# Performance work log

Measured on AMD Instinct MI355X. Metric: run time of the kernel, lower is better.

The kernel has to match this reference:

```python
import jax, jax.numpy as jnp
import numpy as np

N_NODES = 50000
N_EDGES = 800000
D_IN = 128
D_HID = 128
D_OUT = 128


def _sage_conv(x, row, col, Wl, Wr, b):
    # PyG SAGEConv (mean aggregation, root weight, bias):
    # out = mean_{j in N(i)} x_j @ Wl^T + x_i @ Wr^T + b
    n = x.shape[0]
    msg = x[col]                                            # [E, D] gather from source nodes
    agg = jax.ops.segment_sum(msg, row, num_segments=n)     # [N, D]
    deg = jax.ops.segment_sum(jnp.ones((row.shape[0],), x.dtype), row, num_segments=n)
    agg = agg / jnp.maximum(deg, 1.0)[:, None]
    return agg @ Wl.T + x @ Wr.T + b


def setup_inputs() -> dict:
    key = jax.random.key(0)
    ks = jax.random.split(key, 12)
    x = jax.random.normal(ks[0], (N_NODES, D_IN), dtype=jnp.float32)
    edge_row = jax.random.randint(ks[1], (N_EDGES,), 0, N_NODES)
    edge_col = jax.random.randint(ks[2], (N_EDGES,), 0, N_NODES)
    dims = [(D_HID, D_IN), (D_HID, D_HID), (D_OUT, D_HID)]
    inp = {"x": x, "edge_row": edge_row, "edge_col": edge_col}
    for i, (do, di) in enumerate(dims):
        s = 1.0 / np.sqrt(di)
        inp[f"Wl{i}"] = jax.random.uniform(ks[3 + 3 * i], (do, di), jnp.float32, -s, s)
        inp[f"Wr{i}"] = jax.random.uniform(ks[4 + 3 * i], (do, di), jnp.float32, -s, s)
        inp[f"b{i}"] = jax.random.uniform(ks[5 + 3 * i], (do,), jnp.float32, -s, s)
    return inp


def reference(x, edge_row, edge_col, Wl0, Wr0, b0, Wl1, Wr1, b1, Wl2, Wr2, b2):
    # Single branch (num_layers=[3]), use_res=True, dropout=0 (eval mode).
    params = [(Wl0, Wr0, b0), (Wl1, Wr1, b1), (Wl2, Wr2, b2)]
    x1 = _sage_conv(x, edge_row, edge_col, *params[0])
    for Wl, Wr, b in params[1:]:
        x2 = x1
        x1 = jax.nn.relu(x1)
        x1 = _sage_conv(x1, edge_row, edge_col, Wl, Wr, b) + x2
    # x_final = sum(branches) / number; one branch -> divide by 1
    return x1 / 1.0
```

## Files before the change

### kernel.cpp

```cpp
#include <hip/hip_runtime.h>

#define NN 50000
#define NE 800000
#define D  128

typedef _Float16 f16;
typedef _Float16 f16x4 __attribute__((ext_vector_type(4)));
typedef _Float16 f16x8 __attribute__((ext_vector_type(8)));
typedef float f32x4 __attribute__((ext_vector_type(4)));
typedef float f32x2 __attribute__((ext_vector_type(2)));
typedef unsigned short u16;
typedef unsigned int u32;
typedef unsigned char u8;

__global__ __launch_bounds__(256) void prep(
    const float* __restrict__ x, f16* __restrict__ xf, u8* __restrict__ xf8,
    const float* w0, const float* w1, const float* w2,
    const float* w3, const float* w4, const float* w5,
    f16* d0, f16* d1, f16* d2, f16* d3, f16* d4, f16* d5,
    int* __restrict__ deg) {
    int b = blockIdx.x;
    if (b < 6250) {
        int i = b * 256 + threadIdx.x;
        float4 v = ((const float4*)x)[i];
        f16x4 o = {(f16)v.x, (f16)v.y, (f16)v.z, (f16)v.w};
        ((f16x4*)xf)[i] = o;
        u32 lo = __builtin_amdgcn_cvt_pk_fp8_f32(v.x, v.y, 0, false);
        u32 pk = __builtin_amdgcn_cvt_pk_fp8_f32(v.z, v.w, lo, true);
        ((u32*)xf8)[i] = pk;
    } else if (b < 6346) {
        int wb = b - 6250;
        int mat = wb >> 4;
        const float* s; f16* d;
        switch (mat) {
            case 0: s = w0; d = d0; break; case 1: s = w1; d = d1; break;
            case 2: s = w2; d = d2; break; case 3: s = w3; d = d3; break;
            case 4: s = w4; d = d4; break; default: s = w5; d = d5; break;
        }
        int i = (wb & 15) * 256 + threadIdx.x;
        float4 v = ((const float4*)s)[i];
        f16x4 o = {(f16)v.x, (f16)v.y, (f16)v.z, (f16)v.w};
        ((f16x4*)d)[i] = o;
    } else {
        int i = (b - 6346) * 256 + threadIdx.x;
        if (i < NN) deg[i] = 0;
    }
}


__global__ __launch_bounds__(256) void count_deg_rank(
    const int* __restrict__ row, int* __restrict__ deg, u16* __restrict__ rank, int e) {
    int i = blockIdx.x * blockDim.x + threadIdx.x;
    if (i < e) rank[i] = (u16)atomicAdd(&deg[row[i]], 1);
}

__global__ void scan_partial(const int* __restrict__ deg, int* __restrict__ bsum, int n) {
    __shared__ int s[1024];
    int i = blockIdx.x * 1024 + threadIdx.x;
    s[threadIdx.x] = (i < n) ? deg[i] : 0;
    __syncthreads();
    for (int off = 512; off > 0; off >>= 1) {
        if (threadIdx.x < off) s[threadIdx.x] += s[threadIdx.x + off];
        __syncthreads();
    }
    if (threadIdx.x == 0) bsum[blockIdx.x] = s[0];
}

__global__ void scan_final(const int* __restrict__ deg, const int* __restrict__ bsum,
                           int* __restrict__ offsets, int n, int nb) {
    __shared__ int s[1024];
    __shared__ int base;
    if (threadIdx.x < 64) {
        int t = threadIdx.x;
        int v = (t < nb && t < (int)blockIdx.x) ? bsum[t] : 0;
#pragma unroll
        for (int m = 1; m < 64; m <<= 1) v += __shfl_xor(v, m, 64);
        if (t == 0) base = v;
    }
    int i = blockIdx.x * 1024 + threadIdx.x;
    int dv = (i < n) ? deg[i] : 0;
    s[threadIdx.x] = dv;
    __syncthreads();
    for (int off = 1; off < 1024; off <<= 1) {
        int t = (threadIdx.x >= (unsigned)off) ? s[threadIdx.x - off] : 0;
        __syncthreads();
        s[threadIdx.x] += t;
        __syncthreads();
    }
    if (i < n) {
        offsets[i + 1] = s[threadIdx.x] + base;
        if (i == 0) offsets[0] = 0;
    }
}

__global__ __launch_bounds__(256) void fill_csr(
    const int* __restrict__ row, const int* __restrict__ col,
    const u16* __restrict__ rank, const int* __restrict__ offsets,
    u16* __restrict__ csr_col, int e) {
    int i = blockIdx.x * blockDim.x + threadIdx.x;
    if (i < e) {
        int p = offsets[row[i]] + (int)rank[i];
        csr_col[p] = (u16)col[i];
    }
}

__global__ __launch_bounds__(256) void aggregate_f8(
    const u8* __restrict__ h8, const int* __restrict__ offsets,
    const u16* __restrict__ csr, f16* __restrict__ agg) {
    int node = blockIdx.x * 4 + (threadIdx.x >> 6);
    int lane = threadIdx.x & 63;
    int sub = lane >> 4, fl = lane & 15;
    int s0 = offsets[node], e0 = offsets[node + 1];
    int deg = e0 - s0;

    float acc[8];
#pragma unroll
    for (int u = 0; u < 8; ++u) acc[u] = 0.f;

    const u8* hp = h8 + fl * 8;

#define UNPACK_ADD(w)                                                  \
    do {                                                               \
        f32x2 p;                                                       \
        p = __builtin_amdgcn_cvt_pk_f32_fp8((w).x, false);             \
        acc[0] += p.x; acc[1] += p.y;                                  \
        p = __builtin_amdgcn_cvt_pk_f32_fp8((w).x, true);              \
        acc[2] += p.x; acc[3] += p.y;                                  \
        p = __builtin_amdgcn_cvt_pk_f32_fp8((w).y, false);             \
        acc[4] += p.x; acc[5] += p.y;                                  \
        p = __builtin_amdgcn_cvt_pk_f32_fp8((w).y, true);              \
        acc[6] += p.x; acc[7] += p.y;                                  \
    } while (0)

    int j = s0 + sub;
    for (int it = deg >> 3; it > 0; --it, j += 8) {
        int c0 = (int)csr[j];
        int c1 = (int)csr[j + 4];
        uint2 w0 = *(const uint2*)(hp + (size_t)c0 * D);
        uint2 w1 = *(const uint2*)(hp + (size_t)c1 * D);
        UNPACK_ADD(w0);
        UNPACK_ADD(w1);
    }
    if (deg & 4) {
        int c = (int)csr[j];
        uint2 w = *(const uint2*)(hp + (size_t)c * D);
        UNPACK_ADD(w);
        j += 4;
    }
    if (sub < (deg & 3)) {
        int c = (int)csr[j];
        uint2 w = *(const uint2*)(hp + (size_t)c * D);
        UNPACK_ADD(w);
    }
#undef UNPACK_ADD

#pragma unroll
    for (int u = 0; u < 8; ++u) {
        acc[u] += __shfl_xor(acc[u], 16, 64);
        acc[u] += __shfl_xor(acc[u], 32, 64);
    }
    if (sub == 0) {
        float inv = 1.f / fmaxf((float)deg, 1.f);
        f16x8 o;
#pragma unroll
        for (int u = 0; u < 8; ++u) o[u] = (f16)(acc[u] * inv);
        *((f16x8*)(agg + (size_t)node * D) + fl) = o;
    }
}

#define WPAD 72

template<int RELU_X, int ADD_RES, int OUT_F32>
__global__ __launch_bounds__(256, 4) void sage_gemm_mfma(
    const f16* __restrict__ aggb, const f16* __restrict__ xb,
    const f16* __restrict__ Wl, const f16* __restrict__ Wr,
    const float* __restrict__ bias, float* __restrict__ outf,
    f16* __restrict__ outh, u8* __restrict__ out8) {
    __shared__ f16 sW[2][128][WPAD];

    const int tid  = threadIdx.x;
    const int wave = tid >> 6;
    const int lane = tid & 63;
    const int lm = lane & 15;
    const int q  = lane >> 4;
    const int mt = blockIdx.x * 64 + wave * 16;

    int row = mt + lm;
    int rclamp = (row < NN) ? row : NN - 1;

    f16x8 Aa[4], Ax[4];
    const f16* arow = aggb + (size_t)rclamp * D + q * 8;
    const f16* xrow = xb  + (size_t)rclamp * D + q * 8;
#pragma unroll
    for (int ks = 0; ks < 4; ++ks) {
        Aa[ks] = *(const f16x8*)(arow + ks * 32);
        f16x8 v = *(const f16x8*)(xrow + ks * 32);
        if (RELU_X) {
#pragma unroll
            for (int u = 0; u < 8; ++u) v[u] = (v[u] < (f16)0) ? (f16)0 : v[u];
        }
        Ax[ks] = v;
    }

    f32x4 acc[8];
#pragma unroll
    for (int nt = 0; nt < 8; ++nt) acc[nt] = (f32x4){0.f, 0.f, 0.f, 0.f};

    for (int p = 0; p < 2; ++p) {
        __syncthreads();
#pragma unroll
        for (int it = 0; it < 8; ++it) {
            int idx = tid + it * 256;
            int mat = idx >> 10;
            int n   = (idx >> 3) & 127;
            int c   = idx & 7;
            const f16* W = mat ? Wr : Wl;
            f16x8 v = *(const f16x8*)(W + n * D + p * 64 + c * 8);
            *(f16x8*)&sW[mat][n][c * 8] = v;
        }
        __syncthreads();

#pragma unroll
        for (int nt = 0; nt < 8; ++nt) {
#pragma unroll
            for (int k2 = 0; k2 < 2; ++k2) {
                f16x8 bl = *(const f16x8*)&sW[0][nt * 16 + lm][k2 * 32 + q * 8];
                acc[nt] = __builtin_amdgcn_mfma_f32_16x16x32_f16(Aa[p * 2 + k2], bl, acc[nt], 0, 0, 0);
                f16x8 br = *(const f16x8*)&sW[1][nt * 16 + lm][k2 * 32 + q * 8];
                acc[nt] = __builtin_amdgcn_mfma_f32_16x16x32_f16(Ax[p * 2 + k2], br, acc[nt], 0, 0, 0);
            }
        }
    }

#pragma unroll
    for (int nt = 0; nt < 8; ++nt) {
        int n = nt * 16 + lm;
        float bval = bias[n];
#pragma unroll
        for (int r = 0; r < 4; ++r) {
            int m = mt + q * 4 + r;
            if (m < NN) {
                size_t idx = (size_t)m * D + n;
                float v = acc[nt][r] + bval;
                if (ADD_RES) v += (float)xb[idx];
                if (OUT_F32) {
                    outf[idx] = v;
                } else {
                    outh[idx] = (f16)v;
                    u32 t = __builtin_amdgcn_cvt_pk_fp8_f32(fmaxf(v, 0.f), 0.f, 0, false);
                    out8[idx] = (u8)(t & 0xffu);
                }
            }
        }
    }
}


extern "C" void kernel_launch(void* const* d_in, const int* in_sizes, int n_in,
                              void* d_out, int out_size, void* d_ws, size_t ws_size,
                              hipStream_t stream) {
    const float* x    = (const float*)d_in[0];
    const int*   erow = (const int*)d_in[1];
    const int*   ecol = (const int*)d_in[2];
    const float* Wl0 = (const float*)d_in[3];
    const float* Wr0 = (const float*)d_in[4];
    const float* b0  = (const float*)d_in[5];
    const float* Wl1 = (const float*)d_in[6];
    const float* Wr1 = (const float*)d_in[7];
    const float* b1  = (const float*)d_in[8];
    const float* Wl2 = (const float*)d_in[9];
    const float* Wr2 = (const float*)d_in[10];
    const float* b2  = (const float*)d_in[11];

    char* ws = (char*)d_ws;
    size_t off = 0;
    auto carve = [&](size_t bytes) -> void* {
        void* p = ws + off;
        off = (off + bytes + 255) & ~(size_t)255;
        return p;
    };
    int*   deg     = (int*)carve((size_t)NN * 4);
    int*   offsets = (int*)carve((size_t)(NN + 1) * 4);
    int*   bsum    = (int*)carve(64 * 4);
    u16*   rank    = (u16*)carve((size_t)NE * 2);
    u16*   csr_col = (u16*)carve((size_t)NE * 2);
    f16*   xf      = (f16*)carve((size_t)NN * D * 2);
    f16*   x1      = (f16*)carve((size_t)NN * D * 2);
    f16*   aggb    = (f16*)carve((size_t)NN * D * 2);
    u8*    xf8     = (u8*)carve((size_t)NN * D);
    u8*    x1f8    = (u8*)carve((size_t)NN * D);
    f16*   wl0 = (f16*)carve(D * D * 2); f16* wr0 = (f16*)carve(D * D * 2);
    f16*   wl1 = (f16*)carve(D * D * 2); f16* wr1 = (f16*)carve(D * D * 2);
    f16*   wl2 = (f16*)carve(D * D * 2); f16* wr2 = (f16*)carve(D * D * 2);
    (void)ws_size; (void)in_sizes; (void)n_in; (void)out_size;

    float* outp = (float*)d_out;

    prep<<<6542, 256, 0, stream>>>(x, xf, xf8, Wl0, Wr0, Wl1, Wr1, Wl2, Wr2,
                                   wl0, wr0, wl1, wr1, wl2, wr2, deg);

    count_deg_rank<<<(NE + 255) / 256, 256, 0, stream>>>(erow, deg, rank, NE);
    const int nsb = (NN + 1023) / 1024;
    scan_partial<<<nsb, 1024, 0, stream>>>(deg, bsum, NN);
    scan_final<<<nsb, 1024, 0, stream>>>(deg, bsum, offsets, NN, nsb);
    fill_csr<<<(NE + 255) / 256, 256, 0, stream>>>(erow, ecol, rank, offsets, csr_col, NE);

    const int agrid = NN / 4;
    const int ggrid = (NN + 63) / 64;

    aggregate_f8<<<agrid, 256, 0, stream>>>(xf8, offsets, csr_col, aggb);
    sage_gemm_mfma<0, 0, 0><<<ggrid, 256, 0, stream>>>(aggb, xf, wl0, wr0, b0,
                                                       nullptr, x1, x1f8);
    aggregate_f8<<<agrid, 256, 0, stream>>>(x1f8, offsets, csr_col, aggb);
    sage_gemm_mfma<1, 1, 0><<<ggrid, 256, 0, stream>>>(aggb, x1, wl1, wr1, b1,
                                                       nullptr, x1, x1f8);
    aggregate_f8<<<agrid, 256, 0, stream>>>(x1f8, offsets, csr_col, aggb);
    sage_gemm_mfma<1, 1, 1><<<ggrid, 256, 0, stream>>>(aggb, x1, wl2, wr2, b2,
                                                       outp, nullptr, nullptr);
}
```

Before: 277.3 us.

## Fuse neighbor mean aggregation into the SAGE MFMA GEMM kernel

Drops the separate aggregate_f8 kernel and its fp16 agg buffer. Each GEMM wave now gathers the fp8 neighbor rows for its own 16 nodes in registers, divides by degree, and feeds the result straight into the MFMA A operand. The per-layer write and re-read of the aggregate tensor goes away, along with three kernel launches. The fp8 feature buffers ping-pong between layers so gathers never read rows being overwritten. In exchange, each wave loops to the largest degree among its 16 rows, so lanes with smaller degree sit idle. Gather parallelism per node is also lower than in the dedicated aggregation kernel.

```diff
diff --git a/kernel.cpp b/kernel.cpp
--- a/kernel.cpp
+++ b/kernel.cpp
@@ -104,75 +104,12 @@
     }
 }
 
-__global__ __launch_bounds__(256) void aggregate_f8(
+#define WPAD 72
+
+template<int RELU_X, int ADD_RES, int OUT_F32>
+__global__ __launch_bounds__(256, 4) void sage_fused_mfma(
     const u8* __restrict__ h8, const int* __restrict__ offsets,
-    const u16* __restrict__ csr, f16* __restrict__ agg) {
-    int node = blockIdx.x * 4 + (threadIdx.x >> 6);
-    int lane = threadIdx.x & 63;
-    int sub = lane >> 4, fl = lane & 15;
-    int s0 = offsets[node], e0 = offsets[node + 1];
-    int deg = e0 - s0;
-
-    float acc[8];
-#pragma unroll
-    for (int u = 0; u < 8; ++u) acc[u] = 0.f;
-
-    const u8* hp = h8 + fl * 8;
-
-#define UNPACK_ADD(w)                                                  \
-    do {                                                               \
-        f32x2 p;                                                       \
-        p = __builtin_amdgcn_cvt_pk_f32_fp8((w).x, false);             \
-        acc[0] += p.x; acc[1] += p.y;                                  \
-        p = __builtin_amdgcn_cvt_pk_f32_fp8((w).x, true);              \
-        acc[2] += p.x; acc[3] += p.y;                                  \
-        p = __builtin_amdgcn_cvt_pk_f32_fp8((w).y, false);             \
-        acc[4] += p.x; acc[5] += p.y;                                  \
-        p = __builtin_amdgcn_cvt_pk_f32_fp8((w).y, true);              \
-        acc[6] += p.x; acc[7] += p.y;                                  \
-    } while (0)
-
-    int j = s0 + sub;
-    for (int it = deg >> 3; it > 0; --it, j += 8) {
-        int c0 = (int)csr[j];
-        int c1 = (int)csr[j + 4];
-        uint2 w0 = *(const uint2*)(hp + (size_t)c0 * D);
-        uint2 w1 = *(const uint2*)(hp + (size_t)c1 * D);
-        UNPACK_ADD(w0);
-        UNPACK_ADD(w1);
-    }
-    if (deg & 4) {
-        int c = (int)csr[j];
-        uint2 w = *(const uint2*)(hp + (size_t)c * D);
-        UNPACK_ADD(w);
-        j += 4;
-    }
-    if (sub < (deg & 3)) {
-        int c = (int)csr[j];
-        uint2 w = *(const uint2*)(hp + (size_t)c * D);
-        UNPACK_ADD(w);
-    }
-#undef UNPACK_ADD
-
-#pragma unroll
-    for (int u = 0; u < 8; ++u) {
-        acc[u] += __shfl_xor(acc[u], 16, 64);
-        acc[u] += __shfl_xor(acc[u], 32, 64);
-    }
-    if (sub == 0) {
-        float inv = 1.f / fmaxf((float)deg, 1.f);
-        f16x8 o;
-#pragma unroll
-        for (int u = 0; u < 8; ++u) o[u] = (f16)(acc[u] * inv);
-        *((f16x8*)(agg + (size_t)node * D) + fl) = o;
-    }
-}
-
-#define WPAD 72
-
-template<int RELU_X, int ADD_RES, int OUT_F32>
-__global__ __launch_bounds__(256, 4) void sage_gemm_mfma(
-    const f16* __restrict__ aggb, const f16* __restrict__ xb,
+    const u16* __restrict__ csr, const f16* __restrict__ xb,
     const f16* __restrict__ Wl, const f16* __restrict__ Wr,
     const float* __restrict__ bias, float* __restrict__ outf,
     f16* __restrict__ outh, u8* __restrict__ out8) {
@@ -188,12 +125,66 @@
     int row = mt + lm;
     int rclamp = (row < NN) ? row : NN - 1;
 
-    f16x8 Aa[4], Ax[4];
-    const f16* arow = aggb + (size_t)rclamp * D + q * 8;
-    const f16* xrow = xb  + (size_t)rclamp * D + q * 8;
+    int s0  = offsets[rclamp];
+    int deg = offsets[rclamp + 1] - s0;
+
+    float acc_agg[4][8];
+#pragma unroll
+    for (int ks = 0; ks < 4; ++ks)
+#pragma unroll
+        for (int u = 0; u < 8; ++u) acc_agg[ks][u] = 0.f;
+
+    int dmax = deg;
+#pragma unroll
+    for (int m = 1; m < 16; m <<= 1) {
+        int o = __shfl_xor(dmax, m, 64);
+        dmax = (o > dmax) ? o : dmax;
+    }
+
+#define UNPACK_ADD(ks, w)                                              \
+    do {                                                               \
+        f32x2 p;                                                       \
+        p = __builtin_amdgcn_cvt_pk_f32_fp8((w).x, false);             \
+        acc_agg[ks][0] += p.x; acc_agg[ks][1] += p.y;                  \
+        p = __builtin_amdgcn_cvt_pk_f32_fp8((w).x, true);              \
+        acc_agg[ks][2] += p.x; acc_agg[ks][3] += p.y;                  \
+        p = __builtin_amdgcn_cvt_pk_f32_fp8((w).y, false);             \
+        acc_agg[ks][4] += p.x; acc_agg[ks][5] += p.y;                  \
+        p = __builtin_amdgcn_cvt_pk_f32_fp8((w).y, true);              \
+        acc_agg[ks][6] += p.x; acc_agg[ks][7] += p.y;                  \
+    } while (0)
+
+    {
+        const u8* hp = h8 + q * 8;
+        const u16* cp = csr + s0;
+        for (int j = 0; j < dmax; ++j) {
+            if (j < deg) {
+                int c = (int)cp[j];
+                const u8* rp = hp + (c << 7);
+                uint2 w0 = *(const uint2*)(rp);
+                uint2 w1 = *(const uint2*)(rp + 32);
+                uint2 w2 = *(const uint2*)(rp + 64);
+                uint2 w3 = *(const uint2*)(rp + 96);
+                UNPACK_ADD(0, w0);
+                UNPACK_ADD(1, w1);
+                UNPACK_ADD(2, w2);
+                UNPACK_ADD(3, w3);
+            }
+        }
+    }
+#undef UNPACK_ADD
+
+    float inv = 1.f / fmaxf((float)deg, 1.f);
+    f16x8 Aa[4];
+#pragma unroll
+    for (int ks = 0; ks < 4; ++ks)
+#pragma unroll
+        for (int u = 0; u < 8; ++u) Aa[ks][u] = (f16)(acc_agg[ks][u] * inv);
+
+    f16x8 Ax[4];
+    const f16* xrow = xb + (size_t)rclamp * D + q * 8;
 #pragma unroll
     for (int ks = 0; ks < 4; ++ks) {
-        Aa[ks] = *(const f16x8*)(arow + ks * 32);
         f16x8 v = *(const f16x8*)(xrow + ks * 32);
         if (RELU_X) {
 #pragma unroll
@@ -286,7 +277,6 @@
     u16*   csr_col = (u16*)carve((size_t)NE * 2);
     f16*   xf      = (f16*)carve((size_t)NN * D * 2);
     f16*   x1      = (f16*)carve((size_t)NN * D * 2);
-    f16*   aggb    = (f16*)carve((size_t)NN * D * 2);
     u8*    xf8     = (u8*)carve((size_t)NN * D);
     u8*    x1f8    = (u8*)carve((size_t)NN * D);
     f16*   wl0 = (f16*)carve(D * D * 2); f16* wr0 = (f16*)carve(D * D * 2);
@@ -305,16 +295,12 @@
     scan_final<<<nsb, 1024, 0, stream>>>(deg, bsum, offsets, NN, nsb);
     fill_csr<<<(NE + 255) / 256, 256, 0, stream>>>(erow, ecol, rank, offsets, csr_col, NE);
 
-    const int agrid = NN / 4;
     const int ggrid = (NN + 63) / 64;
 
-    aggregate_f8<<<agrid, 256, 0, stream>>>(xf8, offsets, csr_col, aggb);
-    sage_gemm_mfma<0, 0, 0><<<ggrid, 256, 0, stream>>>(aggb, xf, wl0, wr0, b0,
-                                                       nullptr, x1, x1f8);
-    aggregate_f8<<<agrid, 256, 0, stream>>>(x1f8, offsets, csr_col, aggb);
-    sage_gemm_mfma<1, 1, 0><<<ggrid, 256, 0, stream>>>(aggb, x1, wl1, wr1, b1,
-                                                       nullptr, x1, x1f8);
-    aggregate_f8<<<agrid, 256, 0, stream>>>(x1f8, offsets, csr_col, aggb);
-    sage_gemm_mfma<1, 1, 1><<<ggrid, 256, 0, stream>>>(aggb, x1, wl2, wr2, b2,
-                                                       outp, nullptr, nullptr);
-}
+    sage_fused_mfma<0, 0, 0><<<ggrid, 256, 0, stream>>>(
+        xf8, offsets, csr_col, xf, wl0, wr0, b0, nullptr, x1, x1f8);
+    sage_fused_mfma<1, 1, 0><<<ggrid, 256, 0, stream>>>(
+        x1f8, offsets, csr_col, x1, wl1, wr1, b1, nullptr, x1, xf8);
+    sage_fused_mfma<1, 1, 1><<<ggrid, 256, 0, stream>>>(
+        xf8, offsets, csr_col, x1, wl2, wr2, b2, outp, nullptr, nullptr);
+}
```

New measurement: 310.6 us. 1.12x slower.

## Fuse CSR construction into one cooperative kernel and unroll aggregation loop

Applied to the files above, without the earlier changes.

Replaces the four CSR-building launches (degree count, two scan passes, fill) with a single cooperative kernel of 256 blocks of 1024 threads that uses grid-wide syncs between phases, and moves degree zeroing into it. This removes several launch gaps and inter-kernel drains. The cost is fewer threads per phase, so the atomic and fill phases become grid-stride loops, plus the overhead of grid.sync. Separately, the fp8 aggregation inner loop is unrolled to 4 neighbour loads per lane per iteration to raise memory-level parallelism, with an extra remainder step for the deg&8 case.

```diff
diff --git a/kernel.cpp b/kernel.cpp
--- a/kernel.cpp
+++ b/kernel.cpp
@@ -1,4 +1,7 @@
 #include <hip/hip_runtime.h>
+#include <hip/hip_cooperative_groups.h>
+
+namespace cg = cooperative_groups;
 
 #define NN 50000
 #define NE 800000
@@ -17,8 +20,7 @@
     const float* __restrict__ x, f16* __restrict__ xf, u8* __restrict__ xf8,
     const float* w0, const float* w1, const float* w2,
     const float* w3, const float* w4, const float* w5,
-    f16* d0, f16* d1, f16* d2, f16* d3, f16* d4, f16* d5,
-    int* __restrict__ deg) {
+    f16* d0, f16* d1, f16* d2, f16* d3, f16* d4, f16* d5) {
     int b = blockIdx.x;
     if (b < 6250) {
         int i = b * 256 + threadIdx.x;
@@ -28,7 +30,7 @@
         u32 lo = __builtin_amdgcn_cvt_pk_fp8_f32(v.x, v.y, 0, false);
         u32 pk = __builtin_amdgcn_cvt_pk_fp8_f32(v.z, v.w, lo, true);
         ((u32*)xf8)[i] = pk;
-    } else if (b < 6346) {
+    } else {
         int wb = b - 6250;
         int mat = wb >> 4;
         const float* s; f16* d;
@@ -41,66 +43,66 @@
         float4 v = ((const float4*)s)[i];
         f16x4 o = {(f16)v.x, (f16)v.y, (f16)v.z, (f16)v.w};
         ((f16x4*)d)[i] = o;
-    } else {
-        int i = (b - 6346) * 256 + threadIdx.x;
-        if (i < NN) deg[i] = 0;
-    }
-}
-
-
-__global__ __launch_bounds__(256) void count_deg_rank(
-    const int* __restrict__ row, int* __restrict__ deg, u16* __restrict__ rank, int e) {
-    int i = blockIdx.x * blockDim.x + threadIdx.x;
-    if (i < e) rank[i] = (u16)atomicAdd(&deg[row[i]], 1);
-}
-
-__global__ void scan_partial(const int* __restrict__ deg, int* __restrict__ bsum, int n) {
-    __shared__ int s[1024];
-    int i = blockIdx.x * 1024 + threadIdx.x;
-    s[threadIdx.x] = (i < n) ? deg[i] : 0;
-    __syncthreads();
-    for (int off = 512; off > 0; off >>= 1) {
-        if (threadIdx.x < off) s[threadIdx.x] += s[threadIdx.x + off];
-        __syncthreads();
-    }
-    if (threadIdx.x == 0) bsum[blockIdx.x] = s[0];
-}
-
-__global__ void scan_final(const int* __restrict__ deg, const int* __restrict__ bsum,
-                           int* __restrict__ offsets, int n, int nb) {
+    }
+}
+
+__global__ __launch_bounds__(1024) void csr_build(
+    const int* __restrict__ erow, const int* __restrict__ ecol,
+    int* __restrict__ deg, int* __restrict__ bsum, int* __restrict__ offsets,
+    u16* __restrict__ rank, u16* __restrict__ csr_col) {
+    cg::grid_group grid = cg::this_grid();
     __shared__ int s[1024];
     __shared__ int base;
-    if (threadIdx.x < 64) {
-        int t = threadIdx.x;
-        int v = (t < nb && t < (int)blockIdx.x) ? bsum[t] : 0;
-#pragma unroll
-        for (int m = 1; m < 64; m <<= 1) v += __shfl_xor(v, m, 64);
-        if (t == 0) base = v;
-    }
-    int i = blockIdx.x * 1024 + threadIdx.x;
-    int dv = (i < n) ? deg[i] : 0;
-    s[threadIdx.x] = dv;
-    __syncthreads();
-    for (int off = 1; off < 1024; off <<= 1) {
-        int t = (threadIdx.x >= (unsigned)off) ? s[threadIdx.x - off] : 0;
+    const int tid  = threadIdx.x;
+    const int gidx = blockIdx.x * 1024 + tid;
+    const int gsz  = gridDim.x * 1024;
+    const int nsb  = (NN + 1023) / 1024;
+
+    for (int i = gidx; i < NN; i += gsz) deg[i] = 0;
+    grid.sync();
+
+    for (int i = gidx; i < NE; i += gsz) rank[i] = (u16)atomicAdd(&deg[erow[i]], 1);
+    grid.sync();
+
+    if ((int)blockIdx.x < nsb) {
+        int i = blockIdx.x * 1024 + tid;
+        s[tid] = (i < NN) ? deg[i] : 0;
         __syncthreads();
-        s[threadIdx.x] += t;
+        for (int off = 512; off > 0; off >>= 1) {
+            if (tid < off) s[tid] += s[tid + off];
+            __syncthreads();
+        }
+        if (tid == 0) bsum[blockIdx.x] = s[0];
+    }
+    grid.sync();
+
+    if ((int)blockIdx.x < nsb) {
+        if (tid < 64) {
+            int v = (tid < nsb && tid < (int)blockIdx.x) ? bsum[tid] : 0;
+#pragma unroll
+            for (int m = 1; m < 64; m <<= 1) v += __shfl_xor(v, m, 64);
+            if (tid == 0) base = v;
+        }
+        int i = blockIdx.x * 1024 + tid;
+        int dv = (i < NN) ? deg[i] : 0;
+        s[tid] = dv;
         __syncthreads();
-    }
-    if (i < n) {
-        offsets[i + 1] = s[threadIdx.x] + base;
-        if (i == 0) offsets[0] = 0;
-    }
-}
-
-__global__ __launch_bounds__(256) void fill_csr(
-    const int* __restrict__ row, const int* __restrict__ col,
-    const u16* __restrict__ rank, const int* __restrict__ offsets,
-    u16* __restrict__ csr_col, int e) {
-    int i = blockIdx.x * blockDim.x + threadIdx.x;
-    if (i < e) {
-        int p = offsets[row[i]] + (int)rank[i];
-        csr_col[p] = (u16)col[i];
+        for (int off = 1; off < 1024; off <<= 1) {
+            int t = (tid >= off) ? s[tid - off] : 0;
+            __syncthreads();
+            s[tid] += t;
+            __syncthreads();
+        }
+        if (i < NN) {
+            offsets[i + 1] = s[tid] + base;
+            if (i == 0) offsets[0] = 0;
+        }
+    }
+    grid.sync();
+
+    for (int i = gidx; i < NE; i += gsz) {
+        int p = offsets[erow[i]] + (int)rank[i];
+        csr_col[p] = (u16)ecol[i];
     }
 }
 
@@ -133,13 +135,28 @@
     } while (0)
 
     int j = s0 + sub;
-    for (int it = deg >> 3; it > 0; --it, j += 8) {
+    for (int it = deg >> 4; it > 0; --it, j += 16) {
+        int c0 = (int)csr[j];
+        int c1 = (int)csr[j + 4];
+        int c2 = (int)csr[j + 8];
+        int c3 = (int)csr[j + 12];
+        uint2 w0 = *(const uint2*)(hp + (size_t)c0 * D);
+        uint2 w1 = *(const uint2*)(hp + (size_t)c1 * D);
+        uint2 w2 = *(const uint2*)(hp + (size_t)c2 * D);
+        uint2 w3 = *(const uint2*)(hp + (size_t)c3 * D);
+        UNPACK_ADD(w0);
+        UNPACK_ADD(w1);
+        UNPACK_ADD(w2);
+        UNPACK_ADD(w3);
+    }
+    if (deg & 8) {
         int c0 = (int)csr[j];
         int c1 = (int)csr[j + 4];
         uint2 w0 = *(const uint2*)(hp + (size_t)c0 * D);
         uint2 w1 = *(const uint2*)(hp + (size_t)c1 * D);
         UNPACK_ADD(w0);
         UNPACK_ADD(w1);
+        j += 8;
     }
     if (deg & 4) {
         int c = (int)csr[j];
@@ -296,14 +313,15 @@
 
     float* outp = (float*)d_out;
 
-    prep<<<6542, 256, 0, stream>>>(x, xf, xf8, Wl0, Wr0, Wl1, Wr1, Wl2, Wr2,
-                                   wl0, wr0, wl1, wr1, wl2, wr2, deg);
-
-    count_deg_rank<<<(NE + 255) / 256, 256, 0, stream>>>(erow, deg, rank, NE);
-    const int nsb = (NN + 1023) / 1024;
-    scan_partial<<<nsb, 1024, 0, stream>>>(deg, bsum, NN);
-    scan_final<<<nsb, 1024, 0, stream>>>(deg, bsum, offsets, NN, nsb);
-    fill_csr<<<(NE + 255) / 256, 256, 0, stream>>>(erow, ecol, rank, offsets, csr_col, NE);
+    prep<<<6346, 256, 0, stream>>>(x, xf, xf8, Wl0, Wr0, Wl1, Wr1, Wl2, Wr2,
+                                   wl0, wr0, wl1, wr1, wl2, wr2);
+
+    {
+        void* cargs[] = {(void*)&erow, (void*)&ecol, (void*)&deg, (void*)&bsum,
+                         (void*)&offsets, (void*)&rank, (void*)&csr_col};
+        hipLaunchCooperativeKernel((const void*)csr_build, dim3(256), dim3(1024),
+                                   cargs, 0, stream);
+    }
 
     const int agrid = NN / 4;
     const int ggrid = (NN + 63) / 64;
```

Measured after the change: 394.6 us. 42.3% more time.

## Fuse degree counting into prep, single-pass atomic scan, unroll aggregation loop

Applied to the files above, without the earlier changes.

Degree counting and rank assignment move into the prep kernel. The degree array is now zeroed with a memset, and the two-kernel scan becomes a single kernel that takes block bases from an atomic cursor, so the offsets no longer come out in block order. This removes two kernel launches. The aggregation kernel reads degree directly and unrolls its gather loop to four outstanding neighbour loads per iteration, which raises memory-level parallelism at some cost in registers. Because block bases follow atomic arrival order, the CSR layout can change from run to run, but results should stay consistent since each node's offset and degree still match.

```diff
diff --git a/kernel.cpp b/kernel.cpp
--- a/kernel.cpp
+++ b/kernel.cpp
@@ -18,7 +18,7 @@
     const float* w0, const float* w1, const float* w2,
     const float* w3, const float* w4, const float* w5,
     f16* d0, f16* d1, f16* d2, f16* d3, f16* d4, f16* d5,
-    int* __restrict__ deg) {
+    const int* __restrict__ erow, int* __restrict__ deg, u16* __restrict__ rank) {
     int b = blockIdx.x;
     if (b < 6250) {
         int i = b * 256 + threadIdx.x;
@@ -43,54 +43,40 @@
         ((f16x4*)d)[i] = o;
     } else {
         int i = (b - 6346) * 256 + threadIdx.x;
-        if (i < NN) deg[i] = 0;
-    }
-}
-
-
-__global__ __launch_bounds__(256) void count_deg_rank(
-    const int* __restrict__ row, int* __restrict__ deg, u16* __restrict__ rank, int e) {
-    int i = blockIdx.x * blockDim.x + threadIdx.x;
-    if (i < e) rank[i] = (u16)atomicAdd(&deg[row[i]], 1);
-}
-
-__global__ void scan_partial(const int* __restrict__ deg, int* __restrict__ bsum, int n) {
-    __shared__ int s[1024];
-    int i = blockIdx.x * 1024 + threadIdx.x;
-    s[threadIdx.x] = (i < n) ? deg[i] : 0;
+        rank[i] = (u16)atomicAdd(&deg[erow[i]], 1);
+    }
+}
+
+__global__ __launch_bounds__(1024) void scan_offsets(
+    const int* __restrict__ deg, int* __restrict__ cursor,
+    int* __restrict__ offsets) {
+    __shared__ int wsum[16];
+    __shared__ int bbase;
+    const int tid = threadIdx.x;
+    const int w = tid >> 6, lane = tid & 63;
+    const int i = blockIdx.x * 1024 + tid;
+    int v = (i < NN) ? deg[i] : 0;
+    int x = v;
+#pragma unroll
+    for (int m = 1; m < 64; m <<= 1) {
+        int t = __shfl_up(x, m, 64);
+        if (lane >= m) x += t;
+    }
+    if (lane == 63) wsum[w] = x;
     __syncthreads();
-    for (int off = 512; off > 0; off >>= 1) {
-        if (threadIdx.x < off) s[threadIdx.x] += s[threadIdx.x + off];
-        __syncthreads();
-    }
-    if (threadIdx.x == 0) bsum[blockIdx.x] = s[0];
-}
-
-__global__ void scan_final(const int* __restrict__ deg, const int* __restrict__ bsum,
-                           int* __restrict__ offsets, int n, int nb) {
-    __shared__ int s[1024];
-    __shared__ int base;
-    if (threadIdx.x < 64) {
-        int t = threadIdx.x;
-        int v = (t < nb && t < (int)blockIdx.x) ? bsum[t] : 0;
-#pragma unroll
-        for (int m = 1; m < 64; m <<= 1) v += __shfl_xor(v, m, 64);
-        if (t == 0) base = v;
-    }
-    int i = blockIdx.x * 1024 + threadIdx.x;
-    int dv = (i < n) ? deg[i] : 0;
-    s[threadIdx.x] = dv;
+    if (w == 0) {
+        int s = (lane < 16) ? wsum[lane] : 0;
+#pragma unroll
+        for (int m = 1; m < 16; m <<= 1) {
+            int t = __shfl_up(s, m, 64);
+            if (lane >= m) s += t;
+        }
+        if (lane < 16) wsum[lane] = s;
+        if (lane == 15) bbase = atomicAdd(cursor, s);
+    }
     __syncthreads();
-    for (int off = 1; off < 1024; off <<= 1) {
-        int t = (threadIdx.x >= (unsigned)off) ? s[threadIdx.x - off] : 0;
-        __syncthreads();
-        s[threadIdx.x] += t;
-        __syncthreads();
-    }
-    if (i < n) {
-        offsets[i + 1] = s[threadIdx.x] + base;
-        if (i == 0) offsets[0] = 0;
-    }
+    int excl = x - v + (w ? wsum[w - 1] : 0);
+    if (i < NN) offsets[i] = bbase + excl;
 }
 
 __global__ __launch_bounds__(256) void fill_csr(
@@ -106,12 +92,13 @@
 
 __global__ __launch_bounds__(256) void aggregate_f8(
     const u8* __restrict__ h8, const int* __restrict__ offsets,
-    const u16* __restrict__ csr, f16* __restrict__ agg) {
+    const int* __restrict__ degv, const u16* __restrict__ csr,
+    f16* __restrict__ agg) {
     int node = blockIdx.x * 4 + (threadIdx.x >> 6);
     int lane = threadIdx.x & 63;
     int sub = lane >> 4, fl = lane & 15;
-    int s0 = offsets[node], e0 = offsets[node + 1];
-    int deg = e0 - s0;
+    int s0 = offsets[node];
+    int deg = degv[node];
 
     float acc[8];
 #pragma unroll
@@ -133,13 +120,28 @@
     } while (0)
 
     int j = s0 + sub;
-    for (int it = deg >> 3; it > 0; --it, j += 8) {
+    for (int it = deg >> 4; it > 0; --it, j += 16) {
+        int c0 = (int)csr[j];
+        int c1 = (int)csr[j + 4];
+        int c2 = (int)csr[j + 8];
+        int c3 = (int)csr[j + 12];
+        uint2 w0 = *(const uint2*)(hp + (size_t)c0 * D);
+        uint2 w1 = *(const uint2*)(hp + (size_t)c1 * D);
+        uint2 w2 = *(const uint2*)(hp + (size_t)c2 * D);
+        uint2 w3 = *(const uint2*)(hp + (size_t)c3 * D);
+        UNPACK_ADD(w0);
+        UNPACK_ADD(w1);
+        UNPACK_ADD(w2);
+        UNPACK_ADD(w3);
+    }
+    if (deg & 8) {
         int c0 = (int)csr[j];
         int c1 = (int)csr[j + 4];
         uint2 w0 = *(const uint2*)(hp + (size_t)c0 * D);
         uint2 w1 = *(const uint2*)(hp + (size_t)c1 * D);
         UNPACK_ADD(w0);
         UNPACK_ADD(w1);
+        j += 8;
     }
     if (deg & 4) {
         int c = (int)csr[j];
@@ -279,9 +281,8 @@
         off = (off + bytes + 255) & ~(size_t)255;
         return p;
     };
-    int*   deg     = (int*)carve((size_t)NN * 4);
-    int*   offsets = (int*)carve((size_t)(NN + 1) * 4);
-    int*   bsum    = (int*)carve(64 * 4);
+    int*   deg     = (int*)carve((size_t)(NN + 1) * 4);
+    int*   offsets = (int*)carve((size_t)NN * 4);
     u16*   rank    = (u16*)carve((size_t)NE * 2);
     u16*   csr_col = (u16*)carve((size_t)NE * 2);
     f16*   xf      = (f16*)carve((size_t)NN * D * 2);
@@ -296,25 +297,26 @@
 
     float* outp = (float*)d_out;
 
-    prep<<<6542, 256, 0, stream>>>(x, xf, xf8, Wl0, Wr0, Wl1, Wr1, Wl2, Wr2,
-                                   wl0, wr0, wl1, wr1, wl2, wr2, deg);
-
-    count_deg_rank<<<(NE + 255) / 256, 256, 0, stream>>>(erow, deg, rank, NE);
+    hipMemsetAsync(deg, 0, (size_t)(NN + 1) * 4, stream);
+
+    prep<<<9471, 256, 0, stream>>>(x, xf, xf8, Wl0, Wr0, Wl1, Wr1, Wl2, Wr2,
+                                   wl0, wr0, wl1, wr1, wl2, wr2,
+                                   erow, deg, rank);
+
     const int nsb = (NN + 1023) / 1024;
-    scan_partial<<<nsb, 1024, 0, stream>>>(deg, bsum, NN);
-    scan_final<<<nsb, 1024, 0, stream>>>(deg, bsum, offsets, NN, nsb);
+    scan_offsets<<<nsb, 1024, 0, stream>>>(deg, deg + NN, offsets);
     fill_csr<<<(NE + 255) / 256, 256, 0, stream>>>(erow, ecol, rank, offsets, csr_col, NE);
 
     const int agrid = NN / 4;
     const int ggrid = (NN + 63) / 64;
 
-    aggregate_f8<<<agrid, 256, 0, stream>>>(xf8, offsets, csr_col, aggb);
+    aggregate_f8<<<agrid, 256, 0, stream>>>(xf8, offsets, deg, csr_col, aggb);
     sage_gemm_mfma<0, 0, 0><<<ggrid, 256, 0, stream>>>(aggb, xf, wl0, wr0, b0,
                                                        nullptr, x1, x1f8);
-    aggregate_f8<<<agrid, 256, 0, stream>>>(x1f8, offsets, csr_col, aggb);
+    aggregate_f8<<<agrid, 256, 0, stream>>>(x1f8, offsets, deg, csr_col, aggb);
     sage_gemm_mfma<1, 1, 0><<<ggrid, 256, 0, stream>>>(aggb, x1, wl1, wr1, b1,
                                                        nullptr, x1, x1f8);
-    aggregate_f8<<<agrid, 256, 0, stream>>>(x1f8, offsets, csr_col, aggb);
+    aggregate_f8<<<agrid, 256, 0, stream>>>(x1f8, offsets, deg, csr_col, aggb);
     sage_gemm_mfma<1, 1, 1><<<ggrid, 256, 0, stream>>>(aggb, x1, wl2, wr2, b2,
                                                        outp, nullptr, nullptr);
 }
```

Result: faster. 271.8 us (-2.0%).
